# Optimization experiments

Hardware: AMD Instinct MI355X
Metric: run time of the kernel (lower is better)

The kernel has to match this reference:

```python
import jax, jax.numpy as jnp
import numpy as np

WINDOW_SIZE = 11
SIGMA = 1.5
DATA_RANGE = 1.0
CHANNEL = 3
K1 = 0.01
K2 = 0.03
EPS = 1e-08


def _gaussian_window(window_size, sigma, channel):
    # 1D gaussian normalized to sum 1, then outer product -> 2D window
    xs = np.arange(window_size) - window_size // 2
    g = np.exp(-(xs.astype(np.float32) ** 2) / (2.0 * sigma ** 2))
    g = g / g.sum()
    w2d = np.outer(g, g).astype(np.float32)  # [K, K]
    # depthwise kernel in OIHW layout: [channel, 1, K, K]
    return jnp.asarray(np.broadcast_to(w2d, (channel, 1, window_size, window_size)))


def _depthwise_blur(img, window):
    # img: [B, C, H, W], window: [C, 1, K, K]; SAME padding depthwise conv
    pad = WINDOW_SIZE // 2
    return jax.lax.conv_general_dilated(
        img, window,
        window_strides=(1, 1),
        padding=[(pad, pad), (pad, pad)],
        dimension_numbers=("NCHW", "OIHW", "NCHW"),
        feature_group_count=CHANNEL,
    )


def setup_inputs() -> dict:
    key = jax.random.key(0)
    kx, ky = jax.random.split(key)
    x = jax.random.uniform(kx, (32, 3, 512, 512), dtype=jnp.float32)
    y = jax.random.uniform(ky, (32, 3, 512, 512), dtype=jnp.float32)
    return {"x": x, "y": y}


def reference(x, y):
    window = _gaussian_window(WINDOW_SIZE, SIGMA, CHANNEL)
    C1 = (K1 * DATA_RANGE) ** 2
    C2 = (K2 * DATA_RANGE) ** 2

    mu_x = _depthwise_blur(x, window)
    mu_y = _depthwise_blur(y, window)
    mu_x2 = mu_x * mu_x
    mu_y2 = mu_y * mu_y
    mu_xy = mu_x * mu_y

    sigma_x2 = _depthwise_blur(x * x, window) - mu_x2
    sigma_y2 = _depthwise_blur(y * y, window) - mu_y2
    sigma_xy = _depthwise_blur(x * y, window) - mu_xy

    num = (2.0 * mu_xy + C1) * (2.0 * sigma_xy + C2)
    den = (mu_x2 + mu_y2 + C1) * (sigma_x2 + sigma_y2 + C2)
    ssim_map = num / (den + EPS)
    return 1.0 - jnp.mean(ssim_map)
```

## Files before the change

### kernel.cpp

```cpp
#include <hip/hip_runtime.h>

typedef float v4f   __attribute__((ext_vector_type(4)));
typedef float f32x4 __attribute__((ext_vector_type(4)));
typedef _Float16 h4 __attribute__((ext_vector_type(4)));
typedef _Float16 h8 __attribute__((ext_vector_type(8)));

#define HH 512
#define WW 512
#define NPLANES 96
#define NSTRIP 32
#define NBLK (NPLANES * NSTRIP)
#define C1V 1e-4f
#define C2V 9e-4f
#define EPSV 1e-8f
#define NPIX 25165824.0f

#define SLOT_B 768
#define Q_B    3840
#define LDS_B  19200

#define MF(A, B) __builtin_amdgcn_mfma_f32_16x16x32_f16((A), (B), zf, 0, 0, 0)

#define SELW(DST, IX) { const int ix_ = (IX); float r_ = 0.f; \
  r_ = (ix_ == 0) ? wv0 : r_;  r_ = (ix_ == 1) ? wv1 : r_; \
  r_ = (ix_ == 2) ? wv2 : r_;  r_ = (ix_ == 3) ? wv3 : r_; \
  r_ = (ix_ == 4) ? wv4 : r_;  r_ = (ix_ == 5) ? wv5 : r_; \
  r_ = (ix_ == 6) ? wv6 : r_;  r_ = (ix_ == 7) ? wv7 : r_; \
  r_ = (ix_ == 8) ? wv8 : r_;  r_ = (ix_ == 9) ? wv9 : r_; \
  r_ = (ix_ == 10) ? wv10 : r_; DST = r_; }

#define PACK8(DST, F0,F1,F2,F3,F4,F5,F6,F7) \
  DST = (h8){(_Float16)(F0),(_Float16)(F1),(_Float16)(F2),(_Float16)(F3), \
             (_Float16)(F4),(_Float16)(F5),(_Float16)(F6),(_Float16)(F7)};

#define EPX(M) { \
  const float mux_ = mx[M], muy_ = my[M]; \
  const float mx2_ = mux_ * mux_, my2_ = muy_ * muy_, mxy_ = mux_ * muy_; \
  const float sx2_ = vx2[M] - mx2_, sy2_ = vy2[M] - my2_, sxy_ = vxy[M] - mxy_; \
  const float num_ = fmaf(2.f, mxy_, C1V) * fmaf(2.f, sxy_, C2V); \
  const float den_ = (mx2_ + my2_ + C1V) * (sx2_ + sy2_ + C2V) + EPSV; \
  acc = fmaf(num_, __builtin_amdgcn_rcpf(den_), acc); }

#define VSTEP(TAU) { \
  const int tau_ = (TAU); \
  const int ch_ = tau_ - 1 + ((s + 1) >> 1); \
  const int slot_ = ((unsigned)ch_ < 32u) ? (ch_ & 3) : 4; \
  const char* rb_ = lds + slot_ * SLOT_B + rByte; \
  const h8 bx  = *(const h8*)(rb_); \
  const h8 by  = *(const h8*)(rb_ + Q_B); \
  const h8 bx2 = *(const h8*)(rb_ + 2 * Q_B); \
  const h8 by2 = *(const h8*)(rb_ + 3 * Q_B); \
  const h8 bxy = *(const h8*)(rb_ + 4 * Q_B); \
  __builtin_amdgcn_s_setprio(1); \
  const f32x4 mx  = MF(Wf, bx);  const f32x4 my  = MF(Wf, by); \
  const f32x4 vx2 = MF(Wf, bx2); const f32x4 vy2 = MF(Wf, by2); \
  const f32x4 vxy = MF(Wf, bxy); \
  __builtin_amdgcn_s_setprio(0); \
  EPX(0) EPX(1) EPX(2) EPX(3) }

#define STEP(T, CXA,CXB,CYA,CYB, NXA,NXB,NYA,NYB) { \
  const int t_ = (T); \
  if (t_ < 31) { \
    NXA = *(const v4f*)pXa; NXB = *(const v4f*)pXb; \
    NYA = *(const v4f*)pYa; NYB = *(const v4f*)pYb; \
    pXa += 16 * WW; pXb += 16 * WW; pYa += 16 * WW; pYb += 16 * WW; \
  } \
  h8 ax, ay; \
  PACK8(ax, CXA[0],CXA[1],CXA[2],CXA[3], CXB[0],CXB[1],CXB[2],CXB[3]) \
  PACK8(ay, CYA[0],CYA[1],CYA[2],CYA[3], CYB[0],CYB[1],CYB[2],CYB[3]) \
  const h8 ax2 = ax * ax, ay2 = ay * ay, axy = ax * ay; \
  __builtin_amdgcn_s_setprio(1); \
  const f32x4 chx  = MF(ax,  WfH); const f32x4 chy  = MF(ay,  WfH); \
  const f32x4 chx2 = MF(ax2, WfH); const f32x4 chy2 = MF(ay2, WfH); \
  const f32x4 chxy = MF(axy, WfH); \
  __builtin_amdgcn_s_setprio(0); \
  { char* wb_ = lds + (t_ & 3) * SLOT_B + wByte; \
    *(h4*)(wb_)         = (h4){(_Float16)chx[0], (_Float16)chx[1], (_Float16)chx[2], (_Float16)chx[3]}; \
    *(h4*)(wb_ + Q_B)   = (h4){(_Float16)chy[0], (_Float16)chy[1], (_Float16)chy[2], (_Float16)chy[3]}; \
    *(h4*)(wb_ + 2*Q_B) = (h4){(_Float16)chx2[0],(_Float16)chx2[1],(_Float16)chx2[2],(_Float16)chx2[3]}; \
    *(h4*)(wb_ + 3*Q_B) = (h4){(_Float16)chy2[0],(_Float16)chy2[1],(_Float16)chy2[2],(_Float16)chy2[3]}; \
    *(h4*)(wb_ + 4*Q_B) = (h4){(_Float16)chxy[0],(_Float16)chxy[1],(_Float16)chxy[2],(_Float16)chxy[3]}; } \
  if (t_ >= 1) VSTEP(t_ - 1) }

__global__ __launch_bounds__(64)
void ssim_main(const float* __restrict__ x, const float* __restrict__ y,
               float* __restrict__ partial)
{
  __shared__ __attribute__((aligned(16))) char lds[LDS_B];

  const int l = threadIdx.x;
  const int n = l & 15;
  const int s = l >> 4;

  const int wg = blockIdx.x;
  const int swz = (wg & 7) * (NBLK / 8) + (wg >> 3);
  const int plane = swz >> 5;
  const int strip = swz & 31;
  const int C0 = strip * 16;

  const float* xp = x + (size_t)plane * (HH * WW);
  const float* yp = y + (size_t)plane * (HH * WW);

  float wv0, wv1, wv2, wv3, wv4, wv5, wv6, wv7, wv8, wv9, wv10;
#define WINIT(k) wv##k = expf(-((float)((k - 5) * (k - 5))) / 4.5f);
  WINIT(0) WINIT(1) WINIT(2) WINIT(3) WINIT(4) WINIT(5)
  WINIT(6) WINIT(7) WINIT(8) WINIT(9) WINIT(10)
#undef WINIT
  const float inv_ = 1.f / (wv0 + wv1 + wv2 + wv3 + wv4 + wv5 + wv6 + wv7 + wv8 + wv9 + wv10);
#define WNORM(k) wv##k = __int_as_float(__builtin_amdgcn_readfirstlane(__float_as_int(wv##k * inv_)));
  WNORM(0) WNORM(1) WNORM(2) WNORM(3) WNORM(4) WNORM(5)
  WNORM(6) WNORM(7) WNORM(8) WNORM(9) WNORM(10)
#undef WNORM

  const f32x4 zf = {0.f, 0.f, 0.f, 0.f};

  h8 Wf;
  {
    const int kb = 8 * s;
    float b0,b1,b2,b3,b4,b5,b6,b7;
    SELW(b0, kb + 0 - n - 3) SELW(b1, kb + 1 - n - 3)
    SELW(b2, kb + 2 - n - 3) SELW(b3, kb + 3 - n - 3)
    SELW(b4, kb + 4 - n - 3) SELW(b5, kb + 5 - n - 3)
    SELW(b6, kb + 6 - n - 3) SELW(b7, kb + 7 - n - 3)
    PACK8(Wf, b0,b1,b2,b3,b4,b5,b6,b7)
  }

  const int cb = C0 - 8 + 8 * s;
  const bool kill = (cb < 0) || (cb >= WW);
  h8 WfH = Wf;
  if (kill) WfH = (h8)(_Float16)0.f;
  const int ca = kill ? 0 : cb;

  const float* pXa = xp + n * WW + ca;
  const float* pXb = pXa + 4;
  const float* pYa = yp + n * WW + ca;
  const float* pYb = pYa + 4;

  const int wByte = n * 48 + 8 * s;
  const int rByte = n * 48 + 16 * ((s + 1) & 1);

  #pragma unroll
  for (int q = 0; q < 5; ++q)
    #pragma unroll
    for (int j = 0; j < 3; ++j)
      *(unsigned*)(lds + q * Q_B + 4 * SLOT_B + 4 * (l + 64 * j)) = 0u;

  float acc = 0.f;

  v4f XA0 = *(const v4f*)pXa, XB0 = *(const v4f*)pXb;
  v4f YA0 = *(const v4f*)pYa, YB0 = *(const v4f*)pYb;
  pXa += 16 * WW; pXb += 16 * WW; pYa += 16 * WW; pYb += 16 * WW;
  v4f XA1, XB1, YA1, YB1;

  #pragma unroll 1
  for (int u = 0; u < 16; ++u) {
    STEP(2 * u,     XA0, XB0, YA0, YB0,  XA1, XB1, YA1, YB1)
    STEP(2 * u + 1, XA1, XB1, YA1, YB1,  XA0, XB0, YA0, YB0)
  }
  VSTEP(31)

  #pragma unroll
  for (int off = 32; off > 0; off >>= 1) acc += __shfl_down(acc, off);
  if (l == 0) partial[wg] = acc;
}

__global__ void finalize_kernel(const float* __restrict__ partial, float* __restrict__ out)
{
  __shared__ float s4[4];
  float a = 0.f;
  for (int i = threadIdx.x; i < NBLK; i += 256) a += partial[i];
  #pragma unroll
  for (int off = 32; off > 0; off >>= 1) a += __shfl_down(a, off);
  if ((threadIdx.x & 63) == 0) s4[threadIdx.x >> 6] = a;
  __syncthreads();
  if (threadIdx.x == 0) out[0] = 1.f - (s4[0] + s4[1] + s4[2] + s4[3]) * (1.f / NPIX);
}

extern "C" void kernel_launch(void* const* d_in, const int* in_sizes, int n_in,
                              void* d_out, int out_size, void* d_ws, size_t ws_size,
                              hipStream_t stream)
{
  const float* x = (const float*)d_in[0];
  const float* y = (const float*)d_in[1];
  float* ws = (float*)d_ws;
  float* out = (float*)d_out;

  hipLaunchKernelGGL(ssim_main, dim3(NBLK), dim3(64), 0, stream, x, y, ws);
  hipLaunchKernelGGL(finalize_kernel, dim3(1), dim3(256), 0, stream, ws, out);
}
```

Before: 65.82 us.

## Deepen row prefetch and batch horizontal/vertical MFMA steps for more ILP

Reorders the strip loop so that two horizontal-pass steps (even/odd chunks) run back to back, followed by two vertical-pass steps. Global loads are now prefetched two chunks ahead using separate even/odd register sets. The single SSIM accumulator is split into four independent accumulators to break the serial FMA dependency chain. The aim is to hide global-load and MFMA latency within the single-wave workgroup, at the cost of more live vector registers, which may reduce occupancy.

```diff
diff --git a/kernel.cpp b/kernel.cpp
--- a/kernel.cpp
+++ b/kernel.cpp
@@ -39,7 +39,7 @@
   const float sx2_ = vx2[M] - mx2_, sy2_ = vy2[M] - my2_, sxy_ = vxy[M] - mxy_; \
   const float num_ = fmaf(2.f, mxy_, C1V) * fmaf(2.f, sxy_, C2V); \
   const float den_ = (mx2_ + my2_ + C1V) * (sx2_ + sy2_ + C2V) + EPSV; \
-  acc = fmaf(num_, __builtin_amdgcn_rcpf(den_), acc); }
+  acc##M = fmaf(num_, __builtin_amdgcn_rcpf(den_), acc##M); }
 
 #define VSTEP(TAU) { \
   const int tau_ = (TAU); \
@@ -58,9 +58,33 @@
   __builtin_amdgcn_s_setprio(0); \
   EPX(0) EPX(1) EPX(2) EPX(3) }
 
-#define STEP(T, CXA,CXB,CYA,CYB, NXA,NXB,NYA,NYB) { \
+#define HSTEP(T, CXA,CXB,CYA,CYB, NXA,NXB,NYA,NYB) { \
   const int t_ = (T); \
-  if (t_ < 31) { \
+  if (t_ < 30) { \
+    NXA = *(const v4f*)pXa; NXB = *(const v4f*)pXb; \
+    NYA = *(const v4f*)pYa; NYB = *(const v4f*)pYb; \
+    pXa += 16 * WW; pXb += 16 * WW; pYa += 16 * WW; pYb += 16 * WW; \
+  } \
+  h8 ax, ay; \
+  PACK8(ax, CXA[0],CXA[1],CXA[2],CXA[3], CXB[0],CXB[1],CXB[2],CXB[3]) \
+  PACK8(ay, CYA[0],CYA[1],CYA[2],CYA[3], CYB[0],CYB[1],CYB[2],CYB[3]) \
+  const h8 ax2 = ax * ax, ay2 = ay * ay, axy = ax * ay; \
+  __builtin_amdgcn_s_setprio(1); \
+  const f32x4 chx  = MF(ax,  Wf); const f32x4 chy  = MF(ay,  Wf); \
+  const f32x4 chx2 = MF(ax2, Wf); const f32x4 chy2 = MF(ay2, Wf); \
+  const f32x4 chxy = MF(axy, Wf); \
+  __builtin_amdgcn_s_setprio(0); \
+  { char* wb_ = lds + (t_ & 3) * SLOT_B + wByte; \
+    *(h4*)(wb_)         = (h4){(_Float16)chx[0], (_Float16)chx[1], (_Float16)chx[2], (_Float16)chx[3]}; \
+    *(h4*)(wb_ + Q_B)   = (h4){(_Float16)chy[0], (_Float16)chy[1], (_Float16)chy[2], (_Float16)chy[3]}; \
+    *(h4*)(wb_ + 2*Q_B) = (h4){(_Float16)chx2[0],(_Float16)chx2[1],(_Float16)chx2[2],(_Float16)chx2[3]}; \
+    *(h4*)(wb_ + 3*Q_B) = (h4){(_Float16)chy2[0],(_Float16)chy2[1],(_Float16)chy2[2],(_Float16)chy2[3]}; \
+    *(h4*)(wb_ + 4*Q_B) = (h4){(_Float16)chxy[0],(_Float16)chxy[1],(_Float16)chxy[2],(_Float16)chxy[3]}; } }
+
+#undef HSTEP
+#define HSTEP(T, CXA,CXB,CYA,CYB, NXA,NXB,NYA,NYB) { \
+  const int t_ = (T); \
+  if (t_ < 30) { \
     NXA = *(const v4f*)pXa; NXB = *(const v4f*)pXb; \
     NYA = *(const v4f*)pYa; NYB = *(const v4f*)pYb; \
     pXa += 16 * WW; pXb += 16 * WW; pYa += 16 * WW; pYb += 16 * WW; \
@@ -79,8 +103,7 @@
     *(h4*)(wb_ + Q_B)   = (h4){(_Float16)chy[0], (_Float16)chy[1], (_Float16)chy[2], (_Float16)chy[3]}; \
     *(h4*)(wb_ + 2*Q_B) = (h4){(_Float16)chx2[0],(_Float16)chx2[1],(_Float16)chx2[2],(_Float16)chx2[3]}; \
     *(h4*)(wb_ + 3*Q_B) = (h4){(_Float16)chy2[0],(_Float16)chy2[1],(_Float16)chy2[2],(_Float16)chy2[3]}; \
-    *(h4*)(wb_ + 4*Q_B) = (h4){(_Float16)chxy[0],(_Float16)chxy[1],(_Float16)chxy[2],(_Float16)chxy[3]}; } \
-  if (t_ >= 1) VSTEP(t_ - 1) }
+    *(h4*)(wb_ + 4*Q_B) = (h4){(_Float16)chxy[0],(_Float16)chxy[1],(_Float16)chxy[2],(_Float16)chxy[3]}; } }
 
 __global__ __launch_bounds__(64)
 void ssim_main(const float* __restrict__ x, const float* __restrict__ y,
@@ -131,11 +154,6 @@
   if (kill) WfH = (h8)(_Float16)0.f;
   const int ca = kill ? 0 : cb;
 
-  const float* pXa = xp + n * WW + ca;
-  const float* pXb = pXa + 4;
-  const float* pYa = yp + n * WW + ca;
-  const float* pYb = pYa + 4;
-
   const int wByte = n * 48 + 8 * s;
   const int rByte = n * 48 + 16 * ((s + 1) & 1);
 
@@ -145,20 +163,48 @@
     for (int j = 0; j < 3; ++j)
       *(unsigned*)(lds + q * Q_B + 4 * SLOT_B + 4 * (l + 64 * j)) = 0u;
 
-  float acc = 0.f;
-
-  v4f XA0 = *(const v4f*)pXa, XB0 = *(const v4f*)pXb;
-  v4f YA0 = *(const v4f*)pYa, YB0 = *(const v4f*)pYb;
-  pXa += 16 * WW; pXb += 16 * WW; pYa += 16 * WW; pYb += 16 * WW;
-  v4f XA1, XB1, YA1, YB1;
+  float acc0 = 0.f, acc1 = 0.f, acc2 = 0.f, acc3 = 0.f;
+
+  v4f EXA0, EXB0, EYA0, EYB0, EXA1, EXB1, EYA1, EYB1;
+  v4f OXA0, OXB0, OYA0, OYB0, OXA1, OXB1, OYA1, OYB1;
+
+  EXA0 = *(const v4f*)(xp + n * WW + ca);
+  EXB0 = *(const v4f*)(xp + n * WW + ca + 4);
+  EYA0 = *(const v4f*)(yp + n * WW + ca);
+  EYB0 = *(const v4f*)(yp + n * WW + ca + 4);
+  OXA0 = *(const v4f*)(xp + (16 + n) * WW + ca);
+  OXB0 = *(const v4f*)(xp + (16 + n) * WW + ca + 4);
+  OYA0 = *(const v4f*)(yp + (16 + n) * WW + ca);
+  OYB0 = *(const v4f*)(yp + (16 + n) * WW + ca + 4);
+  const float* pXa = xp + (32 + n) * WW + ca;
+  const float* pXb = pXa + 4;
+  const float* pYa = yp + (32 + n) * WW + ca;
+  const float* pYb = pYa + 4;
+
+  HSTEP(0, EXA0,EXB0,EYA0,EYB0, EXA1,EXB1,EYA1,EYB1)
+  HSTEP(1, OXA0,OXB0,OYA0,OYB0, OXA1,OXB1,OYA1,OYB1)
+  VSTEP(0)
 
   #pragma unroll 1
-  for (int u = 0; u < 16; ++u) {
-    STEP(2 * u,     XA0, XB0, YA0, YB0,  XA1, XB1, YA1, YB1)
-    STEP(2 * u + 1, XA1, XB1, YA1, YB1,  XA0, XB0, YA0, YB0)
+  for (int w = 0; w < 7; ++w) {
+    const int u1 = 2 * w + 1;
+    HSTEP(2 * u1,     EXA1,EXB1,EYA1,EYB1, EXA0,EXB0,EYA0,EYB0)
+    HSTEP(2 * u1 + 1, OXA1,OXB1,OYA1,OYB1, OXA0,OXB0,OYA0,OYB0)
+    VSTEP(2 * u1 - 1)
+    VSTEP(2 * u1)
+    const int u2 = 2 * w + 2;
+    HSTEP(2 * u2,     EXA0,EXB0,EYA0,EYB0, EXA1,EXB1,EYA1,EYB1)
+    HSTEP(2 * u2 + 1, OXA0,OXB0,OYA0,OYB0, OXA1,OXB1,OYA1,OYB1)
+    VSTEP(2 * u2 - 1)
+    VSTEP(2 * u2)
   }
+  HSTEP(30, EXA1,EXB1,EYA1,EYB1, EXA0,EXB0,EYA0,EYB0)
+  HSTEP(31, OXA1,OXB1,OYA1,OYB1, OXA0,OXB0,OYA0,OYB0)
+  VSTEP(29)
+  VSTEP(30)
   VSTEP(31)
 
+  float acc = (acc0 + acc1) + (acc2 + acc3);
   #pragma unroll
   for (int off = 32; off > 0; off >>= 1) acc += __shfl_down(acc, off);
   if (l == 0) partial[wg] = acc;
```

New measurement: 60.13 us. 1.09x faster.

## Deepen global prefetch to four row-blocks and batch horizontal/vertical passes

Applied to the files above, without the earlier changes.

Replaces the two-deep register double-buffer with four in-flight row-block loads, widens the LDS ring from 4 to 8 slots, and reorders the loop so four horizontal MFMA steps run in a group interleaved with vertical steps. The per-pixel accumulator is split into four independent chains to shorten the FMA dependency. The aim is to hide global memory latency better in a single-wave workgroup, at the cost of more registers and nearly double the LDS, which may reduce occupancy.

```diff
diff --git a/kernel.cpp b/kernel.cpp
--- a/kernel.cpp
+++ b/kernel.cpp
@@ -16,8 +16,9 @@
 #define NPIX 25165824.0f
 
 #define SLOT_B 768
-#define Q_B    3840
-#define LDS_B  19200
+#define NSLOT  9
+#define Q_B    (NSLOT * SLOT_B)
+#define LDS_B  (5 * Q_B)
 
 #define MF(A, B) __builtin_amdgcn_mfma_f32_16x16x32_f16((A), (B), zf, 0, 0, 0)
 
@@ -39,12 +40,12 @@
   const float sx2_ = vx2[M] - mx2_, sy2_ = vy2[M] - my2_, sxy_ = vxy[M] - mxy_; \
   const float num_ = fmaf(2.f, mxy_, C1V) * fmaf(2.f, sxy_, C2V); \
   const float den_ = (mx2_ + my2_ + C1V) * (sx2_ + sy2_ + C2V) + EPSV; \
-  acc = fmaf(num_, __builtin_amdgcn_rcpf(den_), acc); }
+  acc##M = fmaf(num_, __builtin_amdgcn_rcpf(den_), acc##M); }
 
 #define VSTEP(TAU) { \
   const int tau_ = (TAU); \
   const int ch_ = tau_ - 1 + ((s + 1) >> 1); \
-  const int slot_ = ((unsigned)ch_ < 32u) ? (ch_ & 3) : 4; \
+  const int slot_ = ((unsigned)ch_ < 32u) ? (ch_ & 7) : 8; \
   const char* rb_ = lds + slot_ * SLOT_B + rByte; \
   const h8 bx  = *(const h8*)(rb_); \
   const h8 by  = *(const h8*)(rb_ + Q_B); \
@@ -58,29 +59,28 @@
   __builtin_amdgcn_s_setprio(0); \
   EPX(0) EPX(1) EPX(2) EPX(3) }
 
-#define STEP(T, CXA,CXB,CYA,CYB, NXA,NXB,NYA,NYB) { \
+#define HSTEP(T, CXA,CXB,CYA,CYB) { \
   const int t_ = (T); \
-  if (t_ < 31) { \
-    NXA = *(const v4f*)pXa; NXB = *(const v4f*)pXb; \
-    NYA = *(const v4f*)pYa; NYB = *(const v4f*)pYb; \
-    pXa += 16 * WW; pXb += 16 * WW; pYa += 16 * WW; pYb += 16 * WW; \
-  } \
   h8 ax, ay; \
   PACK8(ax, CXA[0],CXA[1],CXA[2],CXA[3], CXB[0],CXB[1],CXB[2],CXB[3]) \
   PACK8(ay, CYA[0],CYA[1],CYA[2],CYA[3], CYB[0],CYB[1],CYB[2],CYB[3]) \
+  if (t_ < 28) { \
+    CXA = *(const v4f*)pXa; CXB = *(const v4f*)pXb; \
+    CYA = *(const v4f*)pYa; CYB = *(const v4f*)pYb; \
+    pXa += 16 * WW; pXb += 16 * WW; pYa += 16 * WW; pYb += 16 * WW; \
+  } \
   const h8 ax2 = ax * ax, ay2 = ay * ay, axy = ax * ay; \
   __builtin_amdgcn_s_setprio(1); \
   const f32x4 chx  = MF(ax,  WfH); const f32x4 chy  = MF(ay,  WfH); \
   const f32x4 chx2 = MF(ax2, WfH); const f32x4 chy2 = MF(ay2, WfH); \
   const f32x4 chxy = MF(axy, WfH); \
   __builtin_amdgcn_s_setprio(0); \
-  { char* wb_ = lds + (t_ & 3) * SLOT_B + wByte; \
+  { char* wb_ = lds + (t_ & 7) * SLOT_B + wByte; \
     *(h4*)(wb_)         = (h4){(_Float16)chx[0], (_Float16)chx[1], (_Float16)chx[2], (_Float16)chx[3]}; \
     *(h4*)(wb_ + Q_B)   = (h4){(_Float16)chy[0], (_Float16)chy[1], (_Float16)chy[2], (_Float16)chy[3]}; \
     *(h4*)(wb_ + 2*Q_B) = (h4){(_Float16)chx2[0],(_Float16)chx2[1],(_Float16)chx2[2],(_Float16)chx2[3]}; \
     *(h4*)(wb_ + 3*Q_B) = (h4){(_Float16)chy2[0],(_Float16)chy2[1],(_Float16)chy2[2],(_Float16)chy2[3]}; \
-    *(h4*)(wb_ + 4*Q_B) = (h4){(_Float16)chxy[0],(_Float16)chxy[1],(_Float16)chxy[2],(_Float16)chxy[3]}; } \
-  if (t_ >= 1) VSTEP(t_ - 1) }
+    *(h4*)(wb_ + 4*Q_B) = (h4){(_Float16)chxy[0],(_Float16)chxy[1],(_Float16)chxy[2],(_Float16)chxy[3]}; } }
 
 __global__ __launch_bounds__(64)
 void ssim_main(const float* __restrict__ x, const float* __restrict__ y,
@@ -131,11 +131,6 @@
   if (kill) WfH = (h8)(_Float16)0.f;
   const int ca = kill ? 0 : cb;
 
-  const float* pXa = xp + n * WW + ca;
-  const float* pXb = pXa + 4;
-  const float* pYa = yp + n * WW + ca;
-  const float* pYb = pYa + 4;
-
   const int wByte = n * 48 + 8 * s;
   const int rByte = n * 48 + 16 * ((s + 1) & 1);
 
@@ -143,22 +138,57 @@
   for (int q = 0; q < 5; ++q)
     #pragma unroll
     for (int j = 0; j < 3; ++j)
-      *(unsigned*)(lds + q * Q_B + 4 * SLOT_B + 4 * (l + 64 * j)) = 0u;
-
-  float acc = 0.f;
-
-  v4f XA0 = *(const v4f*)pXa, XB0 = *(const v4f*)pXb;
-  v4f YA0 = *(const v4f*)pYa, YB0 = *(const v4f*)pYb;
-  pXa += 16 * WW; pXb += 16 * WW; pYa += 16 * WW; pYb += 16 * WW;
-  v4f XA1, XB1, YA1, YB1;
+      *(unsigned*)(lds + q * Q_B + 8 * SLOT_B + 4 * (l + 64 * j)) = 0u;
+
+  float acc0 = 0.f, acc1 = 0.f, acc2 = 0.f, acc3 = 0.f;
+
+  v4f B0XA, B0XB, B0YA, B0YB, B1XA, B1XB, B1YA, B1YB;
+  v4f B2XA, B2XB, B2YA, B2YB, B3XA, B3XB, B3YA, B3YB;
+
+  B0XA = *(const v4f*)(xp + n * WW + ca);
+  B0XB = *(const v4f*)(xp + n * WW + ca + 4);
+  B0YA = *(const v4f*)(yp + n * WW + ca);
+  B0YB = *(const v4f*)(yp + n * WW + ca + 4);
+  B1XA = *(const v4f*)(xp + (16 + n) * WW + ca);
+  B1XB = *(const v4f*)(xp + (16 + n) * WW + ca + 4);
+  B1YA = *(const v4f*)(yp + (16 + n) * WW + ca);
+  B1YB = *(const v4f*)(yp + (16 + n) * WW + ca + 4);
+  B2XA = *(const v4f*)(xp + (32 + n) * WW + ca);
+  B2XB = *(const v4f*)(xp + (32 + n) * WW + ca + 4);
+  B2YA = *(const v4f*)(yp + (32 + n) * WW + ca);
+  B2YB = *(const v4f*)(yp + (32 + n) * WW + ca + 4);
+  B3XA = *(const v4f*)(xp + (48 + n) * WW + ca);
+  B3XB = *(const v4f*)(xp + (48 + n) * WW + ca + 4);
+  B3YA = *(const v4f*)(yp + (48 + n) * WW + ca);
+  B3YB = *(const v4f*)(yp + (48 + n) * WW + ca + 4);
+  const float* pXa = xp + (64 + n) * WW + ca;
+  const float* pXb = pXa + 4;
+  const float* pYa = yp + (64 + n) * WW + ca;
+  const float* pYb = pYa + 4;
+
+  HSTEP(0, B0XA,B0XB,B0YA,B0YB)
+  HSTEP(1, B1XA,B1XB,B1YA,B1YB)
+  HSTEP(2, B2XA,B2XB,B2YA,B2YB)
+  HSTEP(3, B3XA,B3XB,B3YA,B3YB)
+  VSTEP(0)
 
   #pragma unroll 1
-  for (int u = 0; u < 16; ++u) {
-    STEP(2 * u,     XA0, XB0, YA0, YB0,  XA1, XB1, YA1, YB1)
-    STEP(2 * u + 1, XA1, XB1, YA1, YB1,  XA0, XB0, YA0, YB0)
+  for (int w = 1; w < 8; ++w) {
+    const int t4 = 4 * w;
+    VSTEP(t4 - 3)
+    VSTEP(t4 - 2)
+    HSTEP(t4,     B0XA,B0XB,B0YA,B0YB)
+    HSTEP(t4 + 1, B1XA,B1XB,B1YA,B1YB)
+    HSTEP(t4 + 2, B2XA,B2XB,B2YA,B2YB)
+    HSTEP(t4 + 3, B3XA,B3XB,B3YA,B3YB)
+    VSTEP(t4 - 1)
+    VSTEP(t4)
   }
+  VSTEP(29)
+  VSTEP(30)
   VSTEP(31)
 
+  float acc = (acc0 + acc1) + (acc2 + acc3);
   #pragma unroll
   for (int off = 32; off > 0; off >>= 1) acc += __shfl_down(acc, off);
   if (l == 0) partial[wg] = acc;
```

Measured after the change: 66.00 us. Within noise of the previous version (+0.3%).
